# Kernel tuning notes

Measured on AMD Instinct MI355X. Metric: run time of the kernel, lower is better.

## Reference

```python
import jax, jax.numpy as jnp
import numpy as np

B = 65536
EPS = 1e-5


def _cnot(psi, c, t):
    # psi: [B,2,2,2,2]; qubit q lives on axis q+1. CNOT flips target where control=1.
    c_ax, t_ax = c + 1, t + 1
    p0 = jax.lax.index_in_dim(psi, 0, c_ax, keepdims=True)
    p1 = jax.lax.index_in_dim(psi, 1, c_ax, keepdims=True)
    p1 = jnp.flip(p1, axis=t_ax)
    return jnp.concatenate([p0, p1], axis=c_ax)


def setup_inputs() -> dict:
    key = jax.random.key(0)
    x = jax.random.normal(key, (B, 1, 28, 28), dtype=jnp.float32)
    gamma = jnp.ones((4,), jnp.float32)   # BatchNorm1d(4) weight
    beta = jnp.zeros((4,), jnp.float32)   # BatchNorm1d(4) bias
    return {"x": x, "gamma": gamma, "beta": beta}


def reference(x, gamma, beta):
    bsz = x.shape[0]
    # avg_pool2d(x, 6): kernel=stride=6, no padding -> uses only the top-left 24x24
    pooled = x[:, :, :24, :24].reshape(bsz, 1, 4, 6, 4, 6).mean(axis=(3, 5))
    pooled = pooled.reshape(bsz, 16)
    theta = pooled[:, ::4]  # x[:, i*4] for i=0..3 -> [B,4] RY angles
    half = 0.5 * theta
    q = jnp.stack([jnp.cos(half), jnp.sin(half)], axis=-1)  # [B,4,2], RY|0> amplitudes (real)
    psi = jnp.einsum('bi,bj,bk,bl->bijkl', q[:, 0], q[:, 1], q[:, 2], q[:, 3])
    for c, t in ((0, 1), (1, 2), (2, 3), (3, 0)):
        psi = _cnot(psi, c, t)
    probs = psi * psi  # amplitudes are real
    signs = jnp.array([1.0, -1.0], jnp.float32)
    # <Z_i> = sum_s probs[s] * (-1)^{s_i}
    zs = [jnp.tensordot(probs, signs, axes=[[i + 1], [0]]).sum(axis=(1, 2, 3))
          for i in range(4)]
    out = jnp.stack(zs, axis=1)  # [B,4]
    # BatchNorm1d(4), training mode (biased batch variance)
    mean = out.mean(axis=0)
    var = out.var(axis=0)
    return gamma * (out - mean) / jnp.sqrt(var + EPS) + beta
```

## Files before the change

kernel.cpp:

```cpp
#include <hip/hip_runtime.h>

#define EPS 1e-5f


__global__ __launch_bounds__(256) void qnat_k1(const float* __restrict__ x,
                                               float* __restrict__ z_out,
                                               float* __restrict__ partials,
                                               int bsz) {
    const int t    = threadIdx.x;
    const int lane = t & 63;
    const int w    = t >> 6;
    const int img0 = blockIdx.x * 16 + w * 4;

    const int j1 = 64 + lane, j2 = 128 + lane;
    const int m0 = lane % 7, p0 = lane / 42;
    const int m1 = j1 % 7,   p1 = j1 / 42;
    const int m2 = j2 % 7,   p2 = j2 / 42;

    float s1[4] = {0.f, 0.f, 0.f, 0.f};
    float s2[4] = {0.f, 0.f, 0.f, 0.f};

    #pragma unroll
    for (int pr = 0; pr < 2; ++pr) {
        const int imgA = img0 + pr * 2;
        const int imgB = imgA + 1;

        float4 vA0 = make_float4(0.f,0.f,0.f,0.f), vA1 = vA0, vA2 = vA0;
        float4 vB0 = vA0, vB1 = vA0, vB2 = vA0;
        if (imgA < bsz) {
            const float* ipA = x + (size_t)imgA * 784;
            vA0 = *reinterpret_cast<const float4*>(ipA + 4 * lane);
            vA1 = *reinterpret_cast<const float4*>(ipA + 4 * j1);
            if (lane < 40) vA2 = *reinterpret_cast<const float4*>(ipA + 4 * j2);
        }
        if (imgB < bsz) {
            const float* ipB = x + (size_t)imgB * 784;
            vB0 = *reinterpret_cast<const float4*>(ipB + 4 * lane);
            vB1 = *reinterpret_cast<const float4*>(ipB + 4 * j1);
            if (lane < 40) vB2 = *reinterpret_cast<const float4*>(ipB + 4 * j2);
        }

        float aA0 = 0.f, aA1 = 0.f, aA2 = 0.f, aA3 = 0.f;
        float aB0 = 0.f, aB1 = 0.f, aB2 = 0.f, aB3 = 0.f;
        {
            float h2 = vA0.x + vA0.y, h4 = h2 + vA0.z + vA0.w;
            float c  = (m0 == 0) ? h4 : ((m0 == 1) ? h2 : 0.f);
            aA0 += (p0 == 0) ? c : 0.f; aA1 += (p0 == 1) ? c : 0.f;
            aA2 += (p0 == 2) ? c : 0.f; aA3 += (p0 == 3) ? c : 0.f;
            h2 = vB0.x + vB0.y; h4 = h2 + vB0.z + vB0.w;
            c  = (m0 == 0) ? h4 : ((m0 == 1) ? h2 : 0.f);
            aB0 += (p0 == 0) ? c : 0.f; aB1 += (p0 == 1) ? c : 0.f;
            aB2 += (p0 == 2) ? c : 0.f; aB3 += (p0 == 3) ? c : 0.f;
            h2 = vA1.x + vA1.y; h4 = h2 + vA1.z + vA1.w;
            c  = (m1 == 0) ? h4 : ((m1 == 1) ? h2 : 0.f);
            aA0 += (p1 == 0) ? c : 0.f; aA1 += (p1 == 1) ? c : 0.f;
            aA2 += (p1 == 2) ? c : 0.f; aA3 += (p1 == 3) ? c : 0.f;
            h2 = vB1.x + vB1.y; h4 = h2 + vB1.z + vB1.w;
            c  = (m1 == 0) ? h4 : ((m1 == 1) ? h2 : 0.f);
            aB0 += (p1 == 0) ? c : 0.f; aB1 += (p1 == 1) ? c : 0.f;
            aB2 += (p1 == 2) ? c : 0.f; aB3 += (p1 == 3) ? c : 0.f;
            h2 = vA2.x + vA2.y; h4 = h2 + vA2.z + vA2.w;
            c  = (m2 == 0) ? h4 : ((m2 == 1) ? h2 : 0.f);
            aA0 += (p2 == 0) ? c : 0.f; aA1 += (p2 == 1) ? c : 0.f;
            aA2 += (p2 == 2) ? c : 0.f; aA3 += (p2 == 3) ? c : 0.f;
            h2 = vB2.x + vB2.y; h4 = h2 + vB2.z + vB2.w;
            c  = (m2 == 0) ? h4 : ((m2 == 1) ? h2 : 0.f);
            aB0 += (p2 == 0) ? c : 0.f; aB1 += (p2 == 1) ? c : 0.f;
            aB2 += (p2 == 2) ? c : 0.f; aB3 += (p2 == 3) ? c : 0.f;
        }

        #pragma unroll
        for (int off = 1; off < 64; off <<= 1) {
            aA0 += __shfl_xor(aA0, off, 64);
            aB0 += __shfl_xor(aB0, off, 64);
            aA1 += __shfl_xor(aA1, off, 64);
            aB1 += __shfl_xor(aB1, off, 64);
            aA2 += __shfl_xor(aA2, off, 64);
            aB2 += __shfl_xor(aB2, off, 64);
            aA3 += __shfl_xor(aA3, off, 64);
            aB3 += __shfl_xor(aB3, off, 64);
        }

        const float k = 1.0f / 36.0f;
        const float cA0 = __cosf(aA0 * k), cA1 = __cosf(aA1 * k);
        const float cA2 = __cosf(aA2 * k), cA3 = __cosf(aA3 * k);
        const float cB0 = __cosf(aB0 * k), cB1 = __cosf(aB1 * k);
        const float cB2 = __cosf(aB2 * k), cB3 = __cosf(aB3 * k);

        const float zA1 = cA0 * cA1, zA2 = zA1 * cA2, zA3 = zA2 * cA3, zA0 = cA1 * cA2 * cA3;
        const float zB1 = cB0 * cB1, zB2 = zB1 * cB2, zB3 = zB2 * cB3, zB0 = cB1 * cB2 * cB3;

        if (imgA < bsz) {
            if (lane == 0) {
                float4 zz; zz.x = zA0; zz.y = zA1; zz.z = zA2; zz.w = zA3;
                *reinterpret_cast<float4*>(z_out + (size_t)imgA * 4) = zz;
            }
            s1[0] += zA0; s1[1] += zA1; s1[2] += zA2; s1[3] += zA3;
            s2[0] += zA0*zA0; s2[1] += zA1*zA1; s2[2] += zA2*zA2; s2[3] += zA3*zA3;
        }
        if (imgB < bsz) {
            if (lane == 0) {
                float4 zz; zz.x = zB0; zz.y = zB1; zz.z = zB2; zz.w = zB3;
                *reinterpret_cast<float4*>(z_out + (size_t)imgB * 4) = zz;
            }
            s1[0] += zB0; s1[1] += zB1; s1[2] += zB2; s1[3] += zB3;
            s2[0] += zB0*zB0; s2[1] += zB1*zB1; s2[2] += zB2*zB2; s2[3] += zB3*zB3;
        }
    }

    __shared__ float ps[4][8];
    if (lane == 0) {
        #pragma unroll
        for (int k = 0; k < 4; ++k) { ps[w][k] = s1[k]; ps[w][4 + k] = s2[k]; }
    }
    __syncthreads();
    if (t < 8) {
        partials[blockIdx.x * 8 + t] = (ps[0][t] + ps[1][t]) + (ps[2][t] + ps[3][t]);
    }
}

__global__ __launch_bounds__(256) void qnat_k2(const float* __restrict__ z,
                                               const float* __restrict__ partials,
                                               const float* __restrict__ gamma,
                                               const float* __restrict__ beta,
                                               float* __restrict__ out,
                                               int NB, int bsz) {
    __shared__ float red[4][8];
    __shared__ float st[8];

    const int t = threadIdx.x, lane = t & 63, w = t >> 6;

    float acc[8] = {0.f,0.f,0.f,0.f,0.f,0.f,0.f,0.f};
    for (int r = t; r < NB; r += 256) {
        const float4 a = *reinterpret_cast<const float4*>(partials + r * 8);
        const float4 b = *reinterpret_cast<const float4*>(partials + r * 8 + 4);
        acc[0] += a.x; acc[1] += a.y; acc[2] += a.z; acc[3] += a.w;
        acc[4] += b.x; acc[5] += b.y; acc[6] += b.z; acc[7] += b.w;
    }
    #pragma unroll
    for (int off = 1; off < 64; off <<= 1) {
        #pragma unroll
        for (int k = 0; k < 8; ++k) acc[k] += __shfl_xor(acc[k], off, 64);
    }
    if (lane == 0) {
        #pragma unroll
        for (int k = 0; k < 8; ++k) red[w][k] = acc[k];
    }
    __syncthreads();
    if (t < 8) st[t] = (red[0][t] + red[1][t]) + (red[2][t] + red[3][t]);
    __syncthreads();
    if (t < 4) {
        const double invB = 1.0 / (double)bsz;
        const double m   = (double)st[t] * invB;
        const double var = (double)st[4 + t] * invB - m * m;
        st[t]     = (float)m;
        st[4 + t] = gamma[t] * rsqrtf((float)var + EPS);
    }
    __syncthreads();

    const int img = blockIdx.x * 256 + t;
    if (img < bsz) {
        const float4 zv = reinterpret_cast<const float4*>(z)[img];
        float4 o;
        o.x = (zv.x - st[0]) * st[4] + beta[0];
        o.y = (zv.y - st[1]) * st[5] + beta[1];
        o.z = (zv.z - st[2]) * st[6] + beta[2];
        o.w = (zv.w - st[3]) * st[7] + beta[3];
        reinterpret_cast<float4*>(out)[img] = o;
    }
}

extern "C" void kernel_launch(void* const* d_in, const int* in_sizes, int n_in,
                              void* d_out, int out_size, void* d_ws, size_t ws_size,
                              hipStream_t stream) {
    const float* x     = (const float*)d_in[0];
    const float* gamma = (const float*)d_in[1];
    const float* beta  = (const float*)d_in[2];
    float* out = (float*)d_out;

    const int bsz = in_sizes[0] / 784;
    const int NB  = (bsz + 15) / 16;

    float* z        = (float*)d_ws;
    float* partials = (float*)((char*)d_ws + (size_t)bsz * 16);

    qnat_k1<<<NB, 256, 0, stream>>>(x, z, partials, bsz);
    qnat_k2<<<(bsz + 255) / 256, 256, 0, stream>>>(z, partials, gamma, beta, out, NB, bsz);
}
```

Baseline: 39.87 us.

## Use transpose-style shuffle reduction and distribute per-qubit math across lanes

In the first kernel, the four per-image pooled sums are reduced with a butterfly transpose: the first two shuffle stages exchange partner values, so each lane ends up holding one qubit's sum, and the remaining stages reduce a single value instead of eight. Cosines, z products and BN statistics are then computed per lane for one qubit, which replaces redundant all-lane work with lane-distributed work and extra shuffles. The second kernel now processes four images per thread, cutting its block count and the number of times each block redundantly re-reduces the partials. The cost is more select logic and scalar z stores in place of float4 stores.

```diff
diff --git a/kernel.cpp b/kernel.cpp
--- a/kernel.cpp
+++ b/kernel.cpp
@@ -12,13 +12,16 @@
     const int w    = t >> 6;
     const int img0 = blockIdx.x * 16 + w * 4;
 
+    const bool b0 = (lane & 1) != 0;
+    const bool b1 = (lane & 2) != 0;
+    const int  k  = lane & 3;
+
     const int j1 = 64 + lane, j2 = 128 + lane;
     const int m0 = lane % 7, p0 = lane / 42;
     const int m1 = j1 % 7,   p1 = j1 / 42;
     const int m2 = j2 % 7,   p2 = j2 / 42;
 
-    float s1[4] = {0.f, 0.f, 0.f, 0.f};
-    float s2[4] = {0.f, 0.f, 0.f, 0.f};
+    float s1 = 0.f, s2 = 0.f;
 
     #pragma unroll
     for (int pr = 0; pr < 2; ++pr) {
@@ -51,6 +54,7 @@
             c  = (m0 == 0) ? h4 : ((m0 == 1) ? h2 : 0.f);
             aB0 += (p0 == 0) ? c : 0.f; aB1 += (p0 == 1) ? c : 0.f;
             aB2 += (p0 == 2) ? c : 0.f; aB3 += (p0 == 3) ? c : 0.f;
+
             h2 = vA1.x + vA1.y; h4 = h2 + vA1.z + vA1.w;
             c  = (m1 == 0) ? h4 : ((m1 == 1) ? h2 : 0.f);
             aA0 += (p1 == 0) ? c : 0.f; aA1 += (p1 == 1) ? c : 0.f;
@@ -59,6 +63,7 @@
             c  = (m1 == 0) ? h4 : ((m1 == 1) ? h2 : 0.f);
             aB0 += (p1 == 0) ? c : 0.f; aB1 += (p1 == 1) ? c : 0.f;
             aB2 += (p1 == 2) ? c : 0.f; aB3 += (p1 == 3) ? c : 0.f;
+
             h2 = vA2.x + vA2.y; h4 = h2 + vA2.z + vA2.w;
             c  = (m2 == 0) ? h4 : ((m2 == 1) ? h2 : 0.f);
             aA0 += (p2 == 0) ? c : 0.f; aA1 += (p2 == 1) ? c : 0.f;
@@ -69,50 +74,54 @@
             aB2 += (p2 == 2) ? c : 0.f; aB3 += (p2 == 3) ? c : 0.f;
         }
 
+        float rA = __shfl_xor(b0 ? aA0 : aA1, 1, 64);
+        float rB = __shfl_xor(b0 ? aB0 : aB1, 1, 64);
+        float uA = (b0 ? aA1 : aA0) + rA;
+        float uB = (b0 ? aB1 : aB0) + rB;
+        rA = __shfl_xor(b0 ? aA2 : aA3, 1, 64);
+        rB = __shfl_xor(b0 ? aB2 : aB3, 1, 64);
+        float vA = (b0 ? aA3 : aA2) + rA;
+        float vB = (b0 ? aB3 : aB2) + rB;
+        rA = __shfl_xor(b1 ? uA : vA, 2, 64);
+        rB = __shfl_xor(b1 ? uB : vB, 2, 64);
+        float wA = (b1 ? vA : uA) + rA;
+        float wB = (b1 ? vB : uB) + rB;
         #pragma unroll
-        for (int off = 1; off < 64; off <<= 1) {
-            aA0 += __shfl_xor(aA0, off, 64);
-            aB0 += __shfl_xor(aB0, off, 64);
-            aA1 += __shfl_xor(aA1, off, 64);
-            aB1 += __shfl_xor(aB1, off, 64);
-            aA2 += __shfl_xor(aA2, off, 64);
-            aB2 += __shfl_xor(aB2, off, 64);
-            aA3 += __shfl_xor(aA3, off, 64);
-            aB3 += __shfl_xor(aB3, off, 64);
-        }
-
-        const float k = 1.0f / 36.0f;
-        const float cA0 = __cosf(aA0 * k), cA1 = __cosf(aA1 * k);
-        const float cA2 = __cosf(aA2 * k), cA3 = __cosf(aA3 * k);
-        const float cB0 = __cosf(aB0 * k), cB1 = __cosf(aB1 * k);
-        const float cB2 = __cosf(aB2 * k), cB3 = __cosf(aB3 * k);
-
-        const float zA1 = cA0 * cA1, zA2 = zA1 * cA2, zA3 = zA2 * cA3, zA0 = cA1 * cA2 * cA3;
-        const float zB1 = cB0 * cB1, zB2 = zB1 * cB2, zB3 = zB2 * cB3, zB0 = cB1 * cB2 * cB3;
-
-        if (imgA < bsz) {
-            if (lane == 0) {
-                float4 zz; zz.x = zA0; zz.y = zA1; zz.z = zA2; zz.w = zA3;
-                *reinterpret_cast<float4*>(z_out + (size_t)imgA * 4) = zz;
-            }
-            s1[0] += zA0; s1[1] += zA1; s1[2] += zA2; s1[3] += zA3;
-            s2[0] += zA0*zA0; s2[1] += zA1*zA1; s2[2] += zA2*zA2; s2[3] += zA3*zA3;
-        }
-        if (imgB < bsz) {
-            if (lane == 0) {
-                float4 zz; zz.x = zB0; zz.y = zB1; zz.z = zB2; zz.w = zB3;
-                *reinterpret_cast<float4*>(z_out + (size_t)imgB * 4) = zz;
-            }
-            s1[0] += zB0; s1[1] += zB1; s1[2] += zB2; s1[3] += zB3;
-            s2[0] += zB0*zB0; s2[1] += zB1*zB1; s2[2] += zB2*zB2; s2[3] += zB3*zB3;
-        }
+        for (int off = 4; off < 64; off <<= 1) {
+            wA += __shfl_xor(wA, off, 64);
+            wB += __shfl_xor(wB, off, 64);
+        }
+
+        const float kk = 1.0f / 36.0f;
+        const float cA = __cosf(wA * kk);
+        const float cB = __cosf(wB * kk);
+        const float cm1A = __shfl_xor(cA, 1, 64);
+        const float cm1B = __shfl_xor(cB, 1, 64);
+        const float cm2A = __shfl_xor(cA, 2, 64);
+        const float cm2B = __shfl_xor(cB, 2, 64);
+        const float cm3A = __shfl_xor(cm2A, 1, 64);
+        const float cm3B = __shfl_xor(cm2B, 1, 64);
+
+        const float t3A = cm2A * cm3A, fullA = cm1A * t3A;
+        const float t3B = cm2B * cm3B, fullB = cm1B * t3B;
+        const float zA = (k == 0) ? fullA : (k == 1) ? cA * cm1A
+                       : (k == 2) ? cA * t3A : cA * fullA;
+        const float zB = (k == 0) ? fullB : (k == 1) ? cB * cm1B
+                       : (k == 2) ? cB * t3B : cB * fullB;
+
+        if (lane < 8) {
+            const int  im = (lane < 4) ? imgA : imgB;
+            const float zz = (lane < 4) ? zA : zB;
+            if (im < bsz) z_out[(size_t)im * 4 + k] = zz;
+        }
+        const float zAm = (imgA < bsz) ? zA : 0.f;
+        const float zBm = (imgB < bsz) ? zB : 0.f;
+        s1 += zAm + zBm;
+        s2 += zAm * zAm + zBm * zBm;
     }
 
     __shared__ float ps[4][8];
-    if (lane == 0) {
-        #pragma unroll
-        for (int k = 0; k < 4; ++k) { ps[w][k] = s1[k]; ps[w][4 + k] = s2[k]; }
-    }
+    if (lane < 4) { ps[w][lane] = s1; ps[w][4 + lane] = s2; }
     __syncthreads();
     if (t < 8) {
         partials[blockIdx.x * 8 + t] = (ps[0][t] + ps[1][t]) + (ps[2][t] + ps[3][t]);
@@ -140,11 +149,11 @@
     #pragma unroll
     for (int off = 1; off < 64; off <<= 1) {
         #pragma unroll
-        for (int k = 0; k < 8; ++k) acc[k] += __shfl_xor(acc[k], off, 64);
+        for (int kk = 0; kk < 8; ++kk) acc[kk] += __shfl_xor(acc[kk], off, 64);
     }
     if (lane == 0) {
         #pragma unroll
-        for (int k = 0; k < 8; ++k) red[w][k] = acc[k];
+        for (int kk = 0; kk < 8; ++kk) red[w][kk] = acc[kk];
     }
     __syncthreads();
     if (t < 8) st[t] = (red[0][t] + red[1][t]) + (red[2][t] + red[3][t]);
@@ -158,15 +167,19 @@
     }
     __syncthreads();
 
-    const int img = blockIdx.x * 256 + t;
-    if (img < bsz) {
-        const float4 zv = reinterpret_cast<const float4*>(z)[img];
-        float4 o;
-        o.x = (zv.x - st[0]) * st[4] + beta[0];
-        o.y = (zv.y - st[1]) * st[5] + beta[1];
-        o.z = (zv.z - st[2]) * st[6] + beta[2];
-        o.w = (zv.w - st[3]) * st[7] + beta[3];
-        reinterpret_cast<float4*>(out)[img] = o;
+    const int img0 = blockIdx.x * 1024 + t;
+    #pragma unroll
+    for (int i = 0; i < 4; ++i) {
+        const int img = img0 + i * 256;
+        if (img < bsz) {
+            const float4 zv = reinterpret_cast<const float4*>(z)[img];
+            float4 o;
+            o.x = (zv.x - st[0]) * st[4] + beta[0];
+            o.y = (zv.y - st[1]) * st[5] + beta[1];
+            o.z = (zv.z - st[2]) * st[6] + beta[2];
+            o.w = (zv.w - st[3]) * st[7] + beta[3];
+            reinterpret_cast<float4*>(out)[img] = o;
+        }
     }
 }
 
@@ -180,10 +193,11 @@
 
     const int bsz = in_sizes[0] / 784;
     const int NB  = (bsz + 15) / 16;
+    const int NB2 = (bsz + 1023) / 1024;
 
     float* z        = (float*)d_ws;
     float* partials = (float*)((char*)d_ws + (size_t)bsz * 16);
 
     qnat_k1<<<NB, 256, 0, stream>>>(x, z, partials, bsz);
-    qnat_k2<<<(bsz + 255) / 256, 256, 0, stream>>>(z, partials, gamma, beta, out, NB, bsz);
+    qnat_k2<<<NB2, 256, 0, stream>>>(z, partials, gamma, beta, out, NB, bsz);
 }
```

Result: no change. 39.40 us (-1.2%).
